# Kernel tuning notes

Measured on AMD Instinct MI355X. Metric: run time of the kernel, lower is better.

Reference implementation:

```python
import jax, jax.numpy as jnp
import numpy as np

EPS = 1e-5  # torch.nn.LayerNorm default


def _layer_norm(h, g, b):
    mu = jnp.mean(h, axis=-1, keepdims=True)
    var = jnp.mean(jnp.square(h - mu), axis=-1, keepdims=True)
    return (h - mu) * jax.lax.rsqrt(var + EPS) * g + b


def setup_inputs() -> dict:
    key = jax.random.key(0)
    ks = jax.random.split(key, 16)
    N, E, D, G, H = 100000, 3200000, 16, 64, 8
    x = jax.random.normal(ks[0], (N, D), dtype=jnp.float32)
    edge_index = jax.random.randint(ks[1], (2, E), 0, N, dtype=jnp.int64)
    vp = jax.random.normal(ks[2], (G, D), dtype=jnp.float32)
    batch = jnp.sort(jax.random.randint(ks[3], (N,), 0, G, dtype=jnp.int64))
    def lin(k, fan_in, fan_out):
        bound = 1.0 / np.sqrt(fan_in)
        kw, kb = jax.random.split(k)
        W = jax.random.uniform(kw, (fan_in, fan_out), jnp.float32, -bound, bound)
        b = jax.random.uniform(kb, (fan_out,), jnp.float32, -bound, bound)
        return W, b
    W1, b1 = lin(ks[4], 3 * D, H)
    W2, b2 = lin(ks[5], H, H)
    W3, b3 = lin(ks[6], H, H)
    W4, b4 = lin(ks[7], H, 1)
    g1 = jnp.ones((H,), jnp.float32); be1 = jnp.zeros((H,), jnp.float32)
    g2 = jnp.ones((H,), jnp.float32); be2 = jnp.zeros((H,), jnp.float32)
    g3 = jnp.ones((H,), jnp.float32); be3 = jnp.zeros((H,), jnp.float32)
    return dict(x=x, edge_index=edge_index, vp=vp, batch=batch,
                W1=W1, b1=b1, g1=g1, be1=be1,
                W2=W2, b2=b2, g2=g2, be2=be2,
                W3=W3, b3=b3, g3=g3, be3=be3,
                W4=W4, b4=b4)


def reference(x, edge_index, vp, batch,
              W1, b1, g1, be1, W2, b2, g2, be2, W3, b3, g3, be3, W4, b4):
    start, end = edge_index[0], edge_index[1]
    # gather node features for both endpoints + per-graph features of the start node's event
    edge_inputs = jnp.concatenate([x[start], x[end], vp[batch[start]]], axis=1)  # [E, 3D]
    h = jnp.tanh(_layer_norm(edge_inputs @ W1 + b1, g1, be1))
    h = jnp.tanh(_layer_norm(h @ W2 + b2, g2, be2))
    h = jnp.tanh(_layer_norm(h @ W3 + b3, g3, be3))
    out = h @ W4 + b4  # [E, 1]
    return out.squeeze(-1)
```

## Files before the change

kernel.cpp:

```cpp
#include <hip/hip_runtime.h>
#include <hip/hip_fp16.h>


struct WPack {
    __half2 w2[32];
    __half2 w3[32];
    __half2 b2p[4], b3p[4];
    __half2 g1p[4], be1p[4];
    __half2 g2p[4], be2p[4];
    __half2 g3p[4], be3p[4];
    float w4[8];
    float b4a;
};

typedef __attribute__((ext_vector_type(8))) _Float16 h8;

#if __has_builtin(__builtin_amdgcn_exp2f)
#define EXP2F(x) __builtin_amdgcn_exp2f(x)
#else
#define EXP2F(x) exp2f(x)
#endif

#define K2LOG2E 2.8853900817779268f

__device__ __forceinline__ float fast_tanh(float v) {
    float e = __expf(2.0f * v);
    return fmaf(-2.0f, __builtin_amdgcn_rcpf(e + 1.0f), 1.0f);
}

__global__ __launch_bounds__(256) void node_pre_kernel(
    const float* __restrict__ x,
    const int* __restrict__ batch,
    const float* __restrict__ vp,
    const float* __restrict__ W1,
    const float* __restrict__ b1,
    h8* __restrict__ ya16,
    h8* __restrict__ yb16,
    int N)
{
    int n = blockIdx.x * blockDim.x + threadIdx.x;
    if (n >= N) return;

    const float4* px = reinterpret_cast<const float4*>(x) + (size_t)n * 4;
    float4 x0 = px[0], x1 = px[1], x2 = px[2], x3 = px[3];
    int g = batch[n];
    const float4* pv = reinterpret_cast<const float4*>(vp) + (size_t)g * 4;
    float4 v0 = pv[0], v1 = pv[1], v2 = pv[2], v3 = pv[3];

    float xs[16] = {x0.x, x0.y, x0.z, x0.w, x1.x, x1.y, x1.z, x1.w,
                    x2.x, x2.y, x2.z, x2.w, x3.x, x3.y, x3.z, x3.w};
    float vs[16] = {v0.x, v0.y, v0.z, v0.w, v1.x, v1.y, v1.z, v1.w,
                    v2.x, v2.y, v2.z, v2.w, v3.x, v3.y, v3.z, v3.w};

    float ya[8], yb[8];
#pragma unroll
    for (int j = 0; j < 8; ++j) { ya[j] = b1[j]; yb[j] = 0.0f; }

#pragma unroll
    for (int i = 0; i < 16; ++i) {
        float vx = xs[i];
        float vv = vs[i];
#pragma unroll
        for (int j = 0; j < 8; ++j) {
            ya[j] = fmaf(vx, W1[i * 8 + j], ya[j]);
            ya[j] = fmaf(vv, W1[(32 + i) * 8 + j], ya[j]);
            yb[j] = fmaf(vx, W1[(16 + i) * 8 + j], yb[j]);
        }
    }

    float mua = 0.0f, mub = 0.0f;
#pragma unroll
    for (int j = 0; j < 8; ++j) { mua += ya[j]; mub += yb[j]; }
    mua *= 0.125f; mub *= 0.125f;

    h8 va, vb;
#pragma unroll
    for (int j = 0; j < 8; ++j) {
        va[j] = (_Float16)(ya[j] - mua);
        vb[j] = (_Float16)(yb[j] - mub);
    }
    ya16[n] = va;
    yb16[n] = vb;
}

__global__ void pack_kernel(
    const float* __restrict__ W2, const float* __restrict__ b2,
    const float* __restrict__ W3, const float* __restrict__ b3,
    const float* __restrict__ g1, const float* __restrict__ be1,
    const float* __restrict__ g2, const float* __restrict__ be2,
    const float* __restrict__ g3, const float* __restrict__ be3,
    const float* __restrict__ W4, const float* __restrict__ b4,
    WPack* __restrict__ wp)
{
    if (threadIdx.x != 0 || blockIdx.x != 0) return;
#pragma unroll
    for (int t = 0; t < 32; ++t) {
        wp->w2[t] = __floats2half2_rn(-2.0f * W2[2 * t], -2.0f * W2[2 * t + 1]);
        wp->w3[t] = __floats2half2_rn(-2.0f * W3[2 * t], -2.0f * W3[2 * t + 1]);
    }
    float cs2[8], cs3[8];
#pragma unroll
    for (int j = 0; j < 8; ++j) {
        float s2 = 0.0f, s3 = 0.0f;
#pragma unroll
        for (int i = 0; i < 8; ++i) { s2 += W2[i * 8 + j]; s3 += W3[i * 8 + j]; }
        cs2[j] = b2[j] + s2;
        cs3[j] = b3[j] + s3;
    }
#pragma unroll
    for (int t = 0; t < 4; ++t) {
        wp->b2p[t]  = __floats2half2_rn(cs2[2 * t], cs2[2 * t + 1]);
        wp->b3p[t]  = __floats2half2_rn(cs3[2 * t], cs3[2 * t + 1]);
        wp->g1p[t]  = __floats2half2_rn(K2LOG2E * g1[2 * t],  K2LOG2E * g1[2 * t + 1]);
        wp->be1p[t] = __floats2half2_rn(K2LOG2E * be1[2 * t], K2LOG2E * be1[2 * t + 1]);
        wp->g2p[t]  = __floats2half2_rn(K2LOG2E * g2[2 * t],  K2LOG2E * g2[2 * t + 1]);
        wp->be2p[t] = __floats2half2_rn(K2LOG2E * be2[2 * t], K2LOG2E * be2[2 * t + 1]);
        wp->g3p[t]  = __floats2half2_rn(K2LOG2E * g3[2 * t],  K2LOG2E * g3[2 * t + 1]);
        wp->be3p[t] = __floats2half2_rn(K2LOG2E * be3[2 * t], K2LOG2E * be3[2 * t + 1]);
    }
    float sw4 = 0.0f;
#pragma unroll
    for (int i = 0; i < 8; ++i) { wp->w4[i] = -2.0f * W4[i]; sw4 += W4[i]; }
    wp->b4a = b4[0] + sw4;
}

__device__ __forceinline__ void site_pair(__half2 arg, float& u0, float& u1) {
    float a0 = __low2float(arg);
    float a1 = __high2float(arg);
    u0 = __builtin_amdgcn_rcpf(EXP2F(a0) + 1.0f);
    u1 = __builtin_amdgcn_rcpf(EXP2F(a1) + 1.0f);
}

__global__ __launch_bounds__(256) void edge_main_kernel(
    const int* __restrict__ ei,
    const uint4* __restrict__ ya16,
    const uint4* __restrict__ yb16,
    const WPack* __restrict__ wp,
    float* __restrict__ out, int E)
{
    int tid = blockIdx.x * blockDim.x + threadIdx.x;
    int base = tid * 2;
    if (base >= E) return;

    int s[2], t[2];
    bool dual = (base + 1 < E);
    if (dual) {
        int2 r0 = *reinterpret_cast<const int2*>(ei + base);
        int2 r1 = *reinterpret_cast<const int2*>(ei + E + base);
        s[0] = r0.x; s[1] = r0.y;
        t[0] = r1.x; t[1] = r1.y;
    } else {
        s[0] = ei[base]; t[0] = ei[E + base];
        s[1] = s[0];     t[1] = t[0];
    }

    uint4 ua[2], ub[2];
#pragma unroll
    for (int c = 0; c < 2; ++c) { ua[c] = ya16[s[c]]; ub[c] = yb16[t[c]]; }

    __half2 v[2][4];
#pragma unroll
    for (int c = 0; c < 2; ++c) {
        const __half2* ha = reinterpret_cast<const __half2*>(&ua[c]);
        const __half2* hb2 = reinterpret_cast<const __half2*>(&ub[c]);
#pragma unroll
        for (int k = 0; k < 4; ++k) v[c][k] = __hadd2(ha[k], hb2[k]);
    }

    __half2 rr2[2];
#pragma unroll
    for (int c = 0; c < 2; ++c) {
        __half2 s2 = __hmul2(v[c][0], v[c][0]);
        s2 = __hfma2(v[c][1], v[c][1], s2);
        s2 = __hfma2(v[c][2], v[c][2], s2);
        s2 = __hfma2(v[c][3], v[c][3], s2);
        float ss = __low2float(s2) + __high2float(s2);
        float r = __builtin_amdgcn_rsqf(fmaf(ss, 0.125f, 1e-5f));
        rr2[c] = __floats2half2_rn(r, r);
    }

    __half2 hb[2][8];
#pragma unroll
    for (int c = 0; c < 2; ++c) {
#pragma unroll
        for (int k = 0; k < 4; ++k) {
            __half2 rg  = __hmul2(rr2[c], wp->g1p[k]);
            __half2 arg = __hfma2(v[c][k], rg, wp->be1p[k]);
            float u0, u1;
            site_pair(arg, u0, u1);
            hb[c][2 * k]     = __floats2half2_rn(u0, u0);
            hb[c][2 * k + 1] = __floats2half2_rn(u1, u1);
        }
    }

    __half2 acc[2][4];
#pragma unroll
    for (int c = 0; c < 2; ++c)
#pragma unroll
        for (int k = 0; k < 4; ++k) acc[c][k] = wp->b2p[k];
#pragma unroll
    for (int i = 0; i < 8; ++i) {
#pragma unroll
        for (int c = 0; c < 2; ++c)
#pragma unroll
            for (int k = 0; k < 4; ++k)
                acc[c][k] = __hfma2(hb[c][i], wp->w2[i * 4 + k], acc[c][k]);
    }

#pragma unroll
    for (int c = 0; c < 2; ++c) {
        __half2 sm2 = __hadd2(__hadd2(acc[c][0], acc[c][1]),
                              __hadd2(acc[c][2], acc[c][3]));
        __half2 sq2 = __hmul2(acc[c][0], acc[c][0]);
        sq2 = __hfma2(acc[c][1], acc[c][1], sq2);
        sq2 = __hfma2(acc[c][2], acc[c][2], sq2);
        sq2 = __hfma2(acc[c][3], acc[c][3], sq2);
        float sm = __low2float(sm2) + __high2float(sm2);
        float sq = __low2float(sq2) + __high2float(sq2);
        float mu = sm * 0.125f;
        float var = fmaf(sq, 0.125f, -mu * mu);
        float rr = __builtin_amdgcn_rsqf(var + 1e-5f);
        __half2 rrp = __floats2half2_rn(rr, rr);
        float m = -mu * rr;
        __half2 mm2 = __floats2half2_rn(m, m);
#pragma unroll
        for (int k = 0; k < 4; ++k) {
            __half2 rg  = __hmul2(rrp, wp->g2p[k]);
            __half2 cc  = __hfma2(mm2, wp->g2p[k], wp->be2p[k]);
            __half2 arg = __hfma2(acc[c][k], rg, cc);
            float u0, u1;
            site_pair(arg, u0, u1);
            hb[c][2 * k]     = __floats2half2_rn(u0, u0);
            hb[c][2 * k + 1] = __floats2half2_rn(u1, u1);
        }
    }

#pragma unroll
    for (int c = 0; c < 2; ++c)
#pragma unroll
        for (int k = 0; k < 4; ++k) acc[c][k] = wp->b3p[k];
#pragma unroll
    for (int i = 0; i < 8; ++i) {
#pragma unroll
        for (int c = 0; c < 2; ++c)
#pragma unroll
            for (int k = 0; k < 4; ++k)
                acc[c][k] = __hfma2(hb[c][i], wp->w3[i * 4 + k], acc[c][k]);
    }

    float o[2];
#pragma unroll
    for (int c = 0; c < 2; ++c) {
        __half2 sm2 = __hadd2(__hadd2(acc[c][0], acc[c][1]),
                              __hadd2(acc[c][2], acc[c][3]));
        __half2 sq2 = __hmul2(acc[c][0], acc[c][0]);
        sq2 = __hfma2(acc[c][1], acc[c][1], sq2);
        sq2 = __hfma2(acc[c][2], acc[c][2], sq2);
        sq2 = __hfma2(acc[c][3], acc[c][3], sq2);
        float sm = __low2float(sm2) + __high2float(sm2);
        float sq = __low2float(sq2) + __high2float(sq2);
        float mu = sm * 0.125f;
        float var = fmaf(sq, 0.125f, -mu * mu);
        float rr = __builtin_amdgcn_rsqf(var + 1e-5f);
        __half2 rrp = __floats2half2_rn(rr, rr);
        float m = -mu * rr;
        __half2 mm2 = __floats2half2_rn(m, m);
        float oo = wp->b4a;
#pragma unroll
        for (int k = 0; k < 4; ++k) {
            __half2 rg  = __hmul2(rrp, wp->g3p[k]);
            __half2 cc  = __hfma2(mm2, wp->g3p[k], wp->be3p[k]);
            __half2 arg = __hfma2(acc[c][k], rg, cc);
            float u0, u1;
            site_pair(arg, u0, u1);
            oo = fmaf(u0, wp->w4[2 * k], oo);
            oo = fmaf(u1, wp->w4[2 * k + 1], oo);
        }
        o[c] = oo;
    }

    if (dual) {
        *reinterpret_cast<float2*>(out + base) = make_float2(o[0], o[1]);
    } else {
        out[base] = o[0];
    }
}

__device__ __forceinline__ void ln_tanh8_full(float* h, const float* __restrict__ g,
                                              const float* __restrict__ be) {
    float sm = 0.0f, sq = 0.0f;
#pragma unroll
    for (int j = 0; j < 8; ++j) { sm += h[j]; sq = fmaf(h[j], h[j], sq); }
    float mu = sm * 0.125f;
    float var = fmaf(sq, 0.125f, -mu * mu);
    float rr = __builtin_amdgcn_rsqf(var + 1e-5f);
#pragma unroll
    for (int j = 0; j < 8; ++j)
        h[j] = fast_tanh(fmaf(h[j] - mu, rr * g[j], be[j]));
}

__global__ __launch_bounds__(256) void edge_net_fallback(
    const float* __restrict__ x, const int* __restrict__ ei,
    const float* __restrict__ vp, const int* __restrict__ batch,
    const float* __restrict__ W1, const float* __restrict__ b1,
    const float* __restrict__ g1, const float* __restrict__ be1,
    const float* __restrict__ W2, const float* __restrict__ b2,
    const float* __restrict__ g2, const float* __restrict__ be2,
    const float* __restrict__ W3, const float* __restrict__ b3,
    const float* __restrict__ g3, const float* __restrict__ be3,
    const float* __restrict__ W4, const float* __restrict__ b4,
    float* __restrict__ out, int E)
{
    int e = blockIdx.x * blockDim.x + threadIdx.x;
    if (e >= E) return;
    int s = ei[e], t = ei[E + e];
    int gb = batch[s];
    float in[48];
    const float4* ps = reinterpret_cast<const float4*>(x) + (size_t)s * 4;
    const float4* pt = reinterpret_cast<const float4*>(x) + (size_t)t * 4;
    const float4* pv = reinterpret_cast<const float4*>(vp) + (size_t)gb * 4;
#pragma unroll
    for (int q = 0; q < 4; ++q) {
        float4 a = ps[q];
        in[q*4+0]=a.x; in[q*4+1]=a.y; in[q*4+2]=a.z; in[q*4+3]=a.w;
    }
#pragma unroll
    for (int q = 0; q < 4; ++q) {
        float4 a = pt[q];
        in[16+q*4+0]=a.x; in[16+q*4+1]=a.y; in[16+q*4+2]=a.z; in[16+q*4+3]=a.w;
    }
#pragma unroll
    for (int q = 0; q < 4; ++q) {
        float4 a = pv[q];
        in[32+q*4+0]=a.x; in[32+q*4+1]=a.y; in[32+q*4+2]=a.z; in[32+q*4+3]=a.w;
    }
    float h[8];
#pragma unroll
    for (int j = 0; j < 8; ++j) h[j] = b1[j];
#pragma unroll
    for (int i = 0; i < 48; ++i) {
        float v = in[i];
#pragma unroll
        for (int j = 0; j < 8; ++j) h[j] = fmaf(v, W1[i*8+j], h[j]);
    }
    ln_tanh8_full(h, g1, be1);
    float h2[8];
#pragma unroll
    for (int j = 0; j < 8; ++j) h2[j] = b2[j];
#pragma unroll
    for (int i = 0; i < 8; ++i) {
        float v = h[i];
#pragma unroll
        for (int j = 0; j < 8; ++j) h2[j] = fmaf(v, W2[i*8+j], h2[j]);
    }
    ln_tanh8_full(h2, g2, be2);
    float h3[8];
#pragma unroll
    for (int j = 0; j < 8; ++j) h3[j] = b3[j];
#pragma unroll
    for (int i = 0; i < 8; ++i) {
        float v = h2[i];
#pragma unroll
        for (int j = 0; j < 8; ++j) h3[j] = fmaf(v, W3[i*8+j], h3[j]);
    }
    ln_tanh8_full(h3, g3, be3);
    float o = b4[0];
#pragma unroll
    for (int i = 0; i < 8; ++i) o = fmaf(h3[i], W4[i], o);
    out[e] = o;
}

extern "C" void kernel_launch(void* const* d_in, const int* in_sizes, int n_in,
                              void* d_out, int out_size, void* d_ws, size_t ws_size,
                              hipStream_t stream) {
    const float* x     = (const float*)d_in[0];
    const int*   ei    = (const int*)d_in[1];
    const float* vp    = (const float*)d_in[2];
    const int*   batch = (const int*)d_in[3];
    const float* W1  = (const float*)d_in[4];
    const float* b1  = (const float*)d_in[5];
    const float* g1  = (const float*)d_in[6];
    const float* be1 = (const float*)d_in[7];
    const float* W2  = (const float*)d_in[8];
    const float* b2  = (const float*)d_in[9];
    const float* g2  = (const float*)d_in[10];
    const float* be2 = (const float*)d_in[11];
    const float* W3  = (const float*)d_in[12];
    const float* b3  = (const float*)d_in[13];
    const float* g3  = (const float*)d_in[14];
    const float* be3 = (const float*)d_in[15];
    const float* W4  = (const float*)d_in[16];
    const float* b4  = (const float*)d_in[17];

    int E = in_sizes[1] / 2;
    int N = in_sizes[3];
    float* out = (float*)d_out;

    size_t tab_bytes = (size_t)N * 8 * sizeof(_Float16);
    size_t need = 2 * tab_bytes + sizeof(WPack) + 64;
    if (ws_size >= need) {
        h8* ya16 = (h8*)d_ws;
        h8* yb16 = (h8*)((char*)d_ws + tab_bytes);
        WPack* wp = (WPack*)((char*)d_ws + 2 * tab_bytes);

        int blockA = 256;
        int gridA = (N + blockA - 1) / blockA;
        hipLaunchKernelGGL(node_pre_kernel, dim3(gridA), dim3(blockA), 0, stream,
                           x, batch, vp, W1, b1, ya16, yb16, N);
        hipLaunchKernelGGL(pack_kernel, dim3(1), dim3(64), 0, stream,
                           W2, b2, W3, b3, g1, be1, g2, be2, g3, be3, W4, b4, wp);
        int pairs = (E + 1) / 2;
        int blockB = 256;
        int gridB = (pairs + blockB - 1) / blockB;
        hipLaunchKernelGGL(edge_main_kernel, dim3(gridB), dim3(blockB), 0, stream,
                           ei, (const uint4*)ya16, (const uint4*)yb16, wp, out, E);
    } else {
        int block = 256;
        int grid = (E + block - 1) / block;
        hipLaunchKernelGGL(edge_net_fallback, dim3(grid), dim3(block), 0, stream,
                           x, ei, vp, batch,
                           W1, b1, g1, be1, W2, b2, g2, be2, W3, b3, g3, be3,
                           W4, b4, out, E);
    }
}
```

Before: 149.4 us.

## Process four edges per thread and compute sigmoid in packed half precision

Each thread now handles four edges instead of two, using int4 index loads and float4 stores, with a clamped tail path. The first two layers' tanh-via-sigmoid is now evaluated with packed half2 exp2 and rcp in place of per-lane float transcendentals. This is meant to halve the transcendental instruction count and give each thread more independent gathers in flight. The costs are higher register pressure, which may lower occupancy, and reduced accuracy from fp16 exp2/rcp. The last layer keeps the float path, now calling exp2f directly.

```diff
diff --git a/kernel.cpp b/kernel.cpp
--- a/kernel.cpp
+++ b/kernel.cpp
@@ -14,12 +14,6 @@
 };
 
 typedef __attribute__((ext_vector_type(8))) _Float16 h8;
-
-#if __has_builtin(__builtin_amdgcn_exp2f)
-#define EXP2F(x) __builtin_amdgcn_exp2f(x)
-#else
-#define EXP2F(x) exp2f(x)
-#endif
 
 #define K2LOG2E 2.8853900817779268f
 
@@ -124,11 +118,13 @@
     wp->b4a = b4[0] + sw4;
 }
 
-__device__ __forceinline__ void site_pair(__half2 arg, float& u0, float& u1) {
-    float a0 = __low2float(arg);
-    float a1 = __high2float(arg);
-    u0 = __builtin_amdgcn_rcpf(EXP2F(a0) + 1.0f);
-    u1 = __builtin_amdgcn_rcpf(EXP2F(a1) + 1.0f);
+#define NC 4
+
+__device__ __forceinline__ void site_h2(__half2 arg, __half2& o0, __half2& o1) {
+    __half2 e = h2exp2(arg);
+    __half2 u = h2rcp(__hadd2(e, __float2half2_rn(1.0f)));
+    o0 = __low2half2(u);
+    o1 = __high2half2(u);
 }
 
 __global__ __launch_bounds__(256) void edge_main_kernel(
@@ -139,37 +135,40 @@
     float* __restrict__ out, int E)
 {
     int tid = blockIdx.x * blockDim.x + threadIdx.x;
-    int base = tid * 2;
+    int base = tid * NC;
     if (base >= E) return;
-
-    int s[2], t[2];
-    bool dual = (base + 1 < E);
-    if (dual) {
-        int2 r0 = *reinterpret_cast<const int2*>(ei + base);
-        int2 r1 = *reinterpret_cast<const int2*>(ei + E + base);
-        s[0] = r0.x; s[1] = r0.y;
-        t[0] = r1.x; t[1] = r1.y;
+    bool full = (base + NC - 1 < E);
+
+    int s[NC], t[NC];
+    if (full) {
+        int4 r0 = *reinterpret_cast<const int4*>(ei + base);
+        int4 r1 = *reinterpret_cast<const int4*>(ei + E + base);
+        s[0] = r0.x; s[1] = r0.y; s[2] = r0.z; s[3] = r0.w;
+        t[0] = r1.x; t[1] = r1.y; t[2] = r1.z; t[3] = r1.w;
     } else {
-        s[0] = ei[base]; t[0] = ei[E + base];
-        s[1] = s[0];     t[1] = t[0];
-    }
-
-    uint4 ua[2], ub[2];
-#pragma unroll
-    for (int c = 0; c < 2; ++c) { ua[c] = ya16[s[c]]; ub[c] = yb16[t[c]]; }
-
-    __half2 v[2][4];
-#pragma unroll
-    for (int c = 0; c < 2; ++c) {
+#pragma unroll
+        for (int c = 0; c < NC; ++c) {
+            int e = base + c < E ? base + c : E - 1;
+            s[c] = ei[e]; t[c] = ei[E + e];
+        }
+    }
+
+    uint4 ua[NC], ub[NC];
+#pragma unroll
+    for (int c = 0; c < NC; ++c) { ua[c] = ya16[s[c]]; ub[c] = yb16[t[c]]; }
+
+    __half2 v[NC][4];
+#pragma unroll
+    for (int c = 0; c < NC; ++c) {
         const __half2* ha = reinterpret_cast<const __half2*>(&ua[c]);
-        const __half2* hb2 = reinterpret_cast<const __half2*>(&ub[c]);
-#pragma unroll
-        for (int k = 0; k < 4; ++k) v[c][k] = __hadd2(ha[k], hb2[k]);
-    }
-
-    __half2 rr2[2];
-#pragma unroll
-    for (int c = 0; c < 2; ++c) {
+        const __half2* hbb = reinterpret_cast<const __half2*>(&ub[c]);
+#pragma unroll
+        for (int k = 0; k < 4; ++k) v[c][k] = __hadd2(ha[k], hbb[k]);
+    }
+
+    __half2 rr2[NC];
+#pragma unroll
+    for (int c = 0; c < NC; ++c) {
         __half2 s2 = __hmul2(v[c][0], v[c][0]);
         s2 = __hfma2(v[c][1], v[c][1], s2);
         s2 = __hfma2(v[c][2], v[c][2], s2);
@@ -179,36 +178,33 @@
         rr2[c] = __floats2half2_rn(r, r);
     }
 
-    __half2 hb[2][8];
-#pragma unroll
-    for (int c = 0; c < 2; ++c) {
-#pragma unroll
-        for (int k = 0; k < 4; ++k) {
+    __half2 hb[NC][8];
+#pragma unroll
+    for (int k = 0; k < 4; ++k) {
+#pragma unroll
+        for (int c = 0; c < NC; ++c) {
             __half2 rg  = __hmul2(rr2[c], wp->g1p[k]);
             __half2 arg = __hfma2(v[c][k], rg, wp->be1p[k]);
-            float u0, u1;
-            site_pair(arg, u0, u1);
-            hb[c][2 * k]     = __floats2half2_rn(u0, u0);
-            hb[c][2 * k + 1] = __floats2half2_rn(u1, u1);
+            site_h2(arg, hb[c][2 * k], hb[c][2 * k + 1]);
         }
     }
 
-    __half2 acc[2][4];
-#pragma unroll
-    for (int c = 0; c < 2; ++c)
+    __half2 acc[NC][4];
+#pragma unroll
+    for (int c = 0; c < NC; ++c)
 #pragma unroll
         for (int k = 0; k < 4; ++k) acc[c][k] = wp->b2p[k];
 #pragma unroll
     for (int i = 0; i < 8; ++i) {
 #pragma unroll
-        for (int c = 0; c < 2; ++c)
+        for (int c = 0; c < NC; ++c)
 #pragma unroll
             for (int k = 0; k < 4; ++k)
                 acc[c][k] = __hfma2(hb[c][i], wp->w2[i * 4 + k], acc[c][k]);
     }
 
 #pragma unroll
-    for (int c = 0; c < 2; ++c) {
+    for (int c = 0; c < NC; ++c) {
         __half2 sm2 = __hadd2(__hadd2(acc[c][0], acc[c][1]),
                               __hadd2(acc[c][2], acc[c][3]));
         __half2 sq2 = __hmul2(acc[c][0], acc[c][0]);
@@ -228,29 +224,26 @@
             __half2 rg  = __hmul2(rrp, wp->g2p[k]);
             __half2 cc  = __hfma2(mm2, wp->g2p[k], wp->be2p[k]);
             __half2 arg = __hfma2(acc[c][k], rg, cc);
-            float u0, u1;
-            site_pair(arg, u0, u1);
-            hb[c][2 * k]     = __floats2half2_rn(u0, u0);
-            hb[c][2 * k + 1] = __floats2half2_rn(u1, u1);
+            site_h2(arg, hb[c][2 * k], hb[c][2 * k + 1]);
         }
     }
 
 #pragma unroll
-    for (int c = 0; c < 2; ++c)
+    for (int c = 0; c < NC; ++c)
 #pragma unroll
         for (int k = 0; k < 4; ++k) acc[c][k] = wp->b3p[k];
 #pragma unroll
     for (int i = 0; i < 8; ++i) {
 #pragma unroll
-        for (int c = 0; c < 2; ++c)
+        for (int c = 0; c < NC; ++c)
 #pragma unroll
             for (int k = 0; k < 4; ++k)
                 acc[c][k] = __hfma2(hb[c][i], wp->w3[i * 4 + k], acc[c][k]);
     }
 
-    float o[2];
-#pragma unroll
-    for (int c = 0; c < 2; ++c) {
+    float o[NC];
+#pragma unroll
+    for (int c = 0; c < NC; ++c) {
         __half2 sm2 = __hadd2(__hadd2(acc[c][0], acc[c][1]),
                               __hadd2(acc[c][2], acc[c][3]));
         __half2 sq2 = __hmul2(acc[c][0], acc[c][0]);
@@ -271,18 +264,22 @@
             __half2 rg  = __hmul2(rrp, wp->g3p[k]);
             __half2 cc  = __hfma2(mm2, wp->g3p[k], wp->be3p[k]);
             __half2 arg = __hfma2(acc[c][k], rg, cc);
-            float u0, u1;
-            site_pair(arg, u0, u1);
+            float a0 = __low2float(arg);
+            float a1 = __high2float(arg);
+            float u0 = __builtin_amdgcn_rcpf(exp2f(a0) + 1.0f);
+            float u1 = __builtin_amdgcn_rcpf(exp2f(a1) + 1.0f);
             oo = fmaf(u0, wp->w4[2 * k], oo);
             oo = fmaf(u1, wp->w4[2 * k + 1], oo);
         }
         o[c] = oo;
     }
 
-    if (dual) {
-        *reinterpret_cast<float2*>(out + base) = make_float2(o[0], o[1]);
+    if (full) {
+        *reinterpret_cast<float4*>(out + base) = make_float4(o[0], o[1], o[2], o[3]);
     } else {
-        out[base] = o[0];
+#pragma unroll
+        for (int c = 0; c < NC; ++c)
+            if (base + c < E) out[base + c] = o[c];
     }
 }
 
@@ -409,9 +406,9 @@
                            x, batch, vp, W1, b1, ya16, yb16, N);
         hipLaunchKernelGGL(pack_kernel, dim3(1), dim3(64), 0, stream,
                            W2, b2, W3, b3, g1, be1, g2, be2, g3, be3, W4, b4, wp);
-        int pairs = (E + 1) / 2;
+        int groups = (E + NC - 1) / NC;
         int blockB = 256;
-        int gridB = (pairs + blockB - 1) / blockB;
+        int gridB = (groups + blockB - 1) / blockB;
         hipLaunchKernelGGL(edge_main_kernel, dim3(gridB), dim3(blockB), 0, stream,
                            ei, (const uint4*)ya16, (const uint4*)yb16, wp, out, E);
     } else {
```

New measurement: 144.9 us. -3.0%, faster.
